# Kernel tuning notes

Hardware: AMD Instinct MI355X
Metric: run time of the kernel (lower is better)

The kernel has to match this reference:

```python
import jax, jax.numpy as jnp
import numpy as np

RACE_CYCLE = 1024
BET_AMOUNT = 131072
D1, D2 = 64, 16


def setup_inputs() -> dict:
    key = jax.random.key(0)
    ks = jax.random.split(key, 4)
    s1 = 1.0 / np.sqrt(RACE_CYCLE)
    s2 = 1.0 / np.sqrt(D1)
    s3 = 1.0 / np.sqrt(D2)
    return {
        "inputs": jax.random.normal(ks[0], (RACE_CYCLE, BET_AMOUNT), dtype=jnp.float32),
        "W1": jax.random.normal(ks[1], (RACE_CYCLE, D1), dtype=jnp.float32) * s1,
        "b1": jnp.zeros((D1,), dtype=jnp.float32),
        "W2": jax.random.normal(ks[2], (D1, D2), dtype=jnp.float32) * s2,
        "b2": jnp.zeros((D2,), dtype=jnp.float32),
        "W3": jax.random.normal(ks[3], (D2, 1), dtype=jnp.float32) * s3,
        "b3": jnp.zeros((1,), dtype=jnp.float32),
    }


def reference(inputs, W1, b1, W2, b2, W3, b3):
    # tf.map_fn over transposed rows == one batched MLP over inputs.T
    x = inputs.T                                # [bet_amount, race_cycle]
    h1 = jax.nn.relu(x @ W1 + b1)               # [bet_amount, 64]
    h2 = jax.nn.relu(h1 @ W2 + b2)              # [bet_amount, 16]
    out = (h2 @ W3 + b3)[:, 0]                  # [bet_amount]
    return out[None, :]                         # [1, bet_amount]
```

## Files before the change

### kernel.cpp

```cpp
#include <hip/hip_runtime.h>


#define RC 1024
#define BA 131072
#define D1 64
#define D2 16

#define MB  128
#define KC  64
#define NCH (RC / KC)
#define KS  72
#define HS  68

using f16x8  = __attribute__((ext_vector_type(8))) _Float16;
using f32x16 = __attribute__((ext_vector_type(16))) float;

__global__ __launch_bounds__(256, 4) void mlp3_mfma(
    const float* __restrict__ inputs,
    const float* __restrict__ W1,
    const float* __restrict__ b1,
    const float* __restrict__ W2,
    const float* __restrict__ b2,
    const float* __restrict__ W3,
    const float* __restrict__ b3,
    float* __restrict__ out)
{
    __shared__ __align__(16) _Float16 smem[17408];
    _Float16* Ash = smem;
    _Float16* Wsh = smem + MB * KS;
    float*    Hsh = (float*)smem;

    const int t    = threadIdx.x;
    const int lane = t & 63;
    const int wave = t >> 6;

    const int mA  = t & (MB - 1);
    const int kgA = t >> 7;
    const int nW  = t & 63;
    const int kgW = t >> 6;

    f32x16 acc0 = {};
    f32x16 acc1 = {};

    const int mBase = blockIdx.x * MB;
    const float* Aptr = inputs + mBase + mA;

    for (int c = 0; c < NCH; ++c) {
        const int k0 = c * KC;
        if (c) __syncthreads();

        #pragma unroll
        for (int s = 0; s < 4; ++s) {
            const int kl = s * 16 + kgA * 8;
            float xv[8];
            #pragma unroll
            for (int u = 0; u < 8; ++u)
                xv[u] = Aptr[(size_t)(k0 + kl + u) * BA];
            f16x8 h;
            #pragma unroll
            for (int u = 0; u < 8; ++u) h[u] = (_Float16)xv[u];
            *(f16x8*)(Ash + mA * KS + kl) = h;
        }
        #pragma unroll
        for (int s2 = 0; s2 < 2; ++s2) {
            const int kl = s2 * 32 + kgW * 8;
            float wv[8];
            #pragma unroll
            for (int u = 0; u < 8; ++u)
                wv[u] = W1[(size_t)(k0 + kl + u) * D1 + nW];
            f16x8 h;
            #pragma unroll
            for (int u = 0; u < 8; ++u) h[u] = (_Float16)wv[u];
            *(f16x8*)(Wsh + nW * KS + kl) = h;
        }
        __syncthreads();

        const int mf = wave * 32 + (lane & 31);
        const int kf = (lane >> 5) * 8;
        #pragma unroll
        for (int ks = 0; ks < 4; ++ks) {
            f16x8 a  = *(const f16x8*)(Ash + mf * KS + ks * 16 + kf);
            f16x8 b0f = *(const f16x8*)(Wsh + (lane & 31) * KS + ks * 16 + kf);
            f16x8 b1f = *(const f16x8*)(Wsh + ((lane & 31) + 32) * KS + ks * 16 + kf);
            acc0 = __builtin_amdgcn_mfma_f32_32x32x16_f16(a, b0f, acc0, 0, 0, 0);
            acc1 = __builtin_amdgcn_mfma_f32_32x32x16_f16(a, b1f, acc1, 0, 0, 0);
        }
    }
    __syncthreads();

    float* Hw = Hsh + wave * (32 * HS);
    #pragma unroll
    for (int r = 0; r < 16; ++r) {
        const int mr = (r & 3) + 8 * (r >> 2) + 4 * (lane >> 5);
        Hw[mr * HS + (lane & 31)]      = acc0[r];
        Hw[mr * HS + (lane & 31) + 32] = acc1[r];
    }
    __syncthreads();

    const int mc = lane & 31;
    const float* Hr = Hw + mc * HS;
    float h2[D2];
    #pragma unroll
    for (int e = 0; e < D2; ++e) h2[e] = b2[e];
    #pragma unroll 8
    for (int d = 0; d < D1; ++d) {
        float h = Hr[d] + b1[d];
        h = h > 0.f ? h : 0.f;
        #pragma unroll
        for (int e = 0; e < D2; ++e)
            h2[e] = fmaf(h, W2[d * D2 + e], h2[e]);
    }
    float o = b3[0];
    #pragma unroll
    for (int e = 0; e < D2; ++e) {
        float h = h2[e] > 0.f ? h2[e] : 0.f;
        o = fmaf(h, W3[e], o);
    }
    if (lane < 32)
        out[mBase + wave * 32 + mc] = o;
}

extern "C" void kernel_launch(void* const* d_in, const int* in_sizes, int n_in,
                              void* d_out, int out_size, void* d_ws, size_t ws_size,
                              hipStream_t stream) {
    const float* inputs = (const float*)d_in[0];
    const float* W1     = (const float*)d_in[1];
    const float* b1     = (const float*)d_in[2];
    const float* W2     = (const float*)d_in[3];
    const float* b2     = (const float*)d_in[4];
    const float* W3     = (const float*)d_in[5];
    const float* b3     = (const float*)d_in[6];
    float* out = (float*)d_out;

    dim3 block(256);
    dim3 grid(BA / MB);
    mlp3_mfma<<<grid, block, 0, stream>>>(inputs, W1, b1, W2, b2, W3, b3, out);
}
```

Measured before the change: 681.0 us.

## Load A directly into MFMA registers with double buffering and preload full W1 fragments

The whole W1 is preloaded once per block into LDS, pre-swizzled into MFMA fragment order, so the per-chunk W1 staging and barriers go away. Each wave streams its input rows straight from global memory into registers in the MFMA operand layout, double buffered across k-steps, instead of staging them through shared memory. The block grows to 1024 threads covering 512 rows, and the epilogue splits the 64 hidden units across the two half-waves and combines them with a cross-lane shuffle. In exchange it uses 128 KB of LDS per block, which caps occupancy, and each lane does strided global loads with no LDS reuse.

```diff
diff --git a/kernel.cpp b/kernel.cpp
--- a/kernel.cpp
+++ b/kernel.cpp
@@ -6,16 +6,13 @@
 #define D1 64
 #define D2 16
 
-#define MB  128
-#define KC  64
-#define NCH (RC / KC)
-#define KS  72
-#define HS  68
+#define MB 512
+#define HS 33
 
 using f16x8  = __attribute__((ext_vector_type(8))) _Float16;
 using f32x16 = __attribute__((ext_vector_type(16))) float;
 
-__global__ __launch_bounds__(256, 4) void mlp3_mfma(
+__global__ __launch_bounds__(1024, 4) void mlp3_mfma_v2(
     const float* __restrict__ inputs,
     const float* __restrict__ W1,
     const float* __restrict__ b1,
@@ -25,99 +22,104 @@
     const float* __restrict__ b3,
     float* __restrict__ out)
 {
-    __shared__ __align__(16) _Float16 smem[17408];
-    _Float16* Ash = smem;
-    _Float16* Wsh = smem + MB * KS;
-    float*    Hsh = (float*)smem;
+    __shared__ __align__(16) _Float16 smem[65536];
+    f16x8* Wf = (f16x8*)smem;
 
-    const int t    = threadIdx.x;
-    const int lane = t & 63;
-    const int wave = t >> 6;
+    const int t  = threadIdx.x;
+    const int l  = t & 63;
+    const int wv = t >> 6;
 
-    const int mA  = t & (MB - 1);
-    const int kgA = t >> 7;
-    const int nW  = t & 63;
-    const int kgW = t >> 6;
+    #pragma unroll
+    for (int i = 0; i < 8; ++i) {
+        const int lf   = t + i * 1024;
+        const int lane = lf & 63;
+        const int frag = lf >> 6;
+        const int ks   = frag >> 1;
+        const int nt   = frag & 1;
+        const int n    = (lane & 31) + 32 * nt;
+        const int kb   = ks * 16 + (lane >> 5) * 8;
+        float w8[8];
+        #pragma unroll
+        for (int u = 0; u < 8; ++u) w8[u] = W1[(size_t)(kb + u) * D1 + n];
+        f16x8 h;
+        #pragma unroll
+        for (int u = 0; u < 8; ++u) h[u] = (_Float16)w8[u];
+        Wf[lf] = h;
+    }
+    __syncthreads();
+
+    const int    mrow  = blockIdx.x * MB + wv * 32 + (l & 31);
+    const size_t kstep = (size_t)16 * BA;
+    const float* p0    = inputs + (size_t)((l >> 5) * 8) * BA + mrow;
 
     f32x16 acc0 = {};
     f32x16 acc1 = {};
+    float xa[8], xb[8];
 
-    const int mBase = blockIdx.x * MB;
-    const float* Aptr = inputs + mBase + mA;
+#define LD(X, P) { _Pragma("unroll") \
+    for (int u = 0; u < 8; ++u) X[u] = (P)[(size_t)u * BA]; }
 
-    for (int c = 0; c < NCH; ++c) {
-        const int k0 = c * KC;
-        if (c) __syncthreads();
+#define COMP(X, KS) { \
+    f16x8 a; \
+    _Pragma("unroll") for (int u = 0; u < 8; ++u) a[u] = (_Float16)X[u]; \
+    f16x8 b0f = Wf[(KS) * 128 + l]; \
+    f16x8 b1f = Wf[(KS) * 128 + 64 + l]; \
+    acc0 = __builtin_amdgcn_mfma_f32_32x32x16_f16(a, b0f, acc0, 0, 0, 0); \
+    acc1 = __builtin_amdgcn_mfma_f32_32x32x16_f16(a, b1f, acc1, 0, 0, 0); }
 
-        #pragma unroll
-        for (int s = 0; s < 4; ++s) {
-            const int kl = s * 16 + kgA * 8;
-            float xv[8];
-            #pragma unroll
-            for (int u = 0; u < 8; ++u)
-                xv[u] = Aptr[(size_t)(k0 + kl + u) * BA];
-            f16x8 h;
-            #pragma unroll
-            for (int u = 0; u < 8; ++u) h[u] = (_Float16)xv[u];
-            *(f16x8*)(Ash + mA * KS + kl) = h;
-        }
-        #pragma unroll
-        for (int s2 = 0; s2 < 2; ++s2) {
-            const int kl = s2 * 32 + kgW * 8;
-            float wv[8];
-            #pragma unroll
-            for (int u = 0; u < 8; ++u)
-                wv[u] = W1[(size_t)(k0 + kl + u) * D1 + nW];
-            f16x8 h;
-            #pragma unroll
-            for (int u = 0; u < 8; ++u) h[u] = (_Float16)wv[u];
-            *(f16x8*)(Wsh + nW * KS + kl) = h;
-        }
-        __syncthreads();
+    LD(xa, p0);
+    const float* p = p0 + kstep;
+    for (int ks = 0; ks < 62; ks += 2) {
+        LD(xb, p); p += kstep;
+        COMP(xa, ks);
+        LD(xa, p); p += kstep;
+        COMP(xb, ks + 1);
+    }
+    LD(xb, p);
+    COMP(xa, 62);
+    COMP(xb, 63);
+#undef LD
+#undef COMP
 
-        const int mf = wave * 32 + (lane & 31);
-        const int kf = (lane >> 5) * 8;
-        #pragma unroll
-        for (int ks = 0; ks < 4; ++ks) {
-            f16x8 a  = *(const f16x8*)(Ash + mf * KS + ks * 16 + kf);
-            f16x8 b0f = *(const f16x8*)(Wsh + (lane & 31) * KS + ks * 16 + kf);
-            f16x8 b1f = *(const f16x8*)(Wsh + ((lane & 31) + 32) * KS + ks * 16 + kf);
-            acc0 = __builtin_amdgcn_mfma_f32_32x32x16_f16(a, b0f, acc0, 0, 0, 0);
-            acc1 = __builtin_amdgcn_mfma_f32_32x32x16_f16(a, b1f, acc1, 0, 0, 0);
-        }
-    }
     __syncthreads();
+    float* Hw = (float*)smem + wv * (32 * HS);
+    const int mc = l & 31;
+    const int dh = l >> 5;
 
-    float* Hw = Hsh + wave * (32 * HS);
-    #pragma unroll
-    for (int r = 0; r < 16; ++r) {
-        const int mr = (r & 3) + 8 * (r >> 2) + 4 * (lane >> 5);
-        Hw[mr * HS + (lane & 31)]      = acc0[r];
-        Hw[mr * HS + (lane & 31) + 32] = acc1[r];
-    }
-    __syncthreads();
-
-    const int mc = lane & 31;
-    const float* Hr = Hw + mc * HS;
     float h2[D2];
     #pragma unroll
-    for (int e = 0; e < D2; ++e) h2[e] = b2[e];
-    #pragma unroll 8
-    for (int d = 0; d < D1; ++d) {
-        float h = Hr[d] + b1[d];
-        h = h > 0.f ? h : 0.f;
-        #pragma unroll
-        for (int e = 0; e < D2; ++e)
-            h2[e] = fmaf(h, W2[d * D2 + e], h2[e]);
-    }
+    for (int e = 0; e < D2; ++e) h2[e] = (dh == 0) ? b2[e] : 0.f;
+
+#define EPI(ACC, DBASE) { \
+    _Pragma("unroll") for (int r = 0; r < 16; ++r) { \
+        const int mr = (r & 3) + 8 * (r >> 2) + 4 * dh; \
+        Hw[mr * HS + mc] = ACC[r]; \
+    } \
+    asm volatile("s_waitcnt lgkmcnt(0)" ::: "memory"); \
+    _Pragma("unroll") for (int dd = 0; dd < 16; ++dd) { \
+        const int d = (DBASE) + dh * 16 + dd; \
+        float h = Hw[mc * HS + dh * 16 + dd] + b1[d]; \
+        h = h > 0.f ? h : 0.f; \
+        _Pragma("unroll") for (int e = 0; e < D2; ++e) \
+            h2[e] = fmaf(h, W2[d * D2 + e], h2[e]); \
+    } \
+    asm volatile("s_waitcnt lgkmcnt(0)" ::: "memory"); }
+
+    EPI(acc0, 0)
+    EPI(acc1, 32)
+#undef EPI
+
+    #pragma unroll
+    for (int e = 0; e < D2; ++e) h2[e] += __shfl_xor(h2[e], 32, 64);
+
     float o = b3[0];
     #pragma unroll
     for (int e = 0; e < D2; ++e) {
         float h = h2[e] > 0.f ? h2[e] : 0.f;
         o = fmaf(h, W3[e], o);
     }
-    if (lane < 32)
-        out[mBase + wave * 32 + mc] = o;
+    if (l < 32)
+        out[blockIdx.x * MB + wv * 32 + mc] = o;
 }
 
 extern "C" void kernel_launch(void* const* d_in, const int* in_sizes, int n_in,
@@ -132,7 +134,7 @@
     const float* b3     = (const float*)d_in[6];
     float* out = (float*)d_out;
 
-    dim3 block(256);
+    dim3 block(1024);
     dim3 grid(BA / MB);
-    mlp3_mfma<<<grid, block, 0, stream>>>(inputs, W1, b1, W2, b2, W3, b3, out);
+    mlp3_mfma_v2<<<grid, block, 0, stream>>>(inputs, W1, b1, W2, b2, W3, b3, out);
 }
```

Result: slower. 715.5 us (+5.1%).
